# Performance work log

Measured on AMD Instinct MI355X. Metric: run time of the kernel, lower is better.

Reference implementation:

```python
import jax, jax.numpy as jnp
import numpy as np

H = 1024          # hidden_size
RH = 2 * H        # router/expert hidden (hidden_multiplier=2)
E = 3             # num_experts
B, T, P = 8, 2048, 64
LN_EPS = 1e-5


def _layer_norm(x, gamma, beta):
    mu = jnp.mean(x, axis=-1, keepdims=True)
    var = jnp.mean(jnp.square(x - mu), axis=-1, keepdims=True)
    return (x - mu) * jax.lax.rsqrt(var + LN_EPS) * gamma + beta


def setup_inputs() -> dict:
    key = jax.random.key(0)
    ks = jax.random.split(key, 24)
    s = lambda fan_in: 1.0 / np.sqrt(fan_in)
    inp = {
        "mix_hidden_states": jax.random.normal(ks[0], (B, T, H), jnp.float32),
        "global_anchor": jax.random.normal(ks[1], (B, H), jnp.float32),
        "prototype_bank": jax.random.normal(ks[2], (B, P, H), jnp.float32),
        # LayerNorm
        "ln_gamma": jnp.ones((H,), jnp.float32),
        "ln_beta": jnp.zeros((H,), jnp.float32),
        # retriever (no bias)
        "Wq": jax.random.normal(ks[3], (H, H), jnp.float32) * s(H),
        "Wk": jax.random.normal(ks[4], (H, H), jnp.float32) * s(H),
        "Wv": jax.random.normal(ks[5], (H, H), jnp.float32) * s(H),
        # router linear: 3H -> E
        "router_W": jax.random.normal(ks[6], (3 * H, E), jnp.float32) * s(3 * H),
        "router_b": jnp.zeros((E,), jnp.float32),
        # experts stacked: [E, 3H, RH] and [E, RH, H]
        "e_w1": jax.random.normal(ks[7], (E, 3 * H, RH), jnp.float32) * s(3 * H),
        "e_b1": jnp.zeros((E, RH), jnp.float32),
        "e_w2": jax.random.normal(ks[8], (E, RH, H), jnp.float32) * s(RH),
        "e_b2": jnp.zeros((E, H), jnp.float32),
        # gate MLP: 3H -> H -> H
        "gate_w1": jax.random.normal(ks[9], (3 * H, H), jnp.float32) * s(3 * H),
        "gate_b1": jnp.zeros((H,), jnp.float32),
        "gate_w2": jax.random.normal(ks[10], (H, H), jnp.float32) * s(H),
        "gate_b2": jnp.zeros((H,), jnp.float32),
        # out_proj (zero-init in torch, but use random for nontrivial baseline)
        "out_w": jax.random.normal(ks[11], (H, H), jnp.float32) * s(H),
        "out_b": jnp.zeros((H,), jnp.float32),
    }
    return inp


def reference(mix_hidden_states, global_anchor, prototype_bank,
              ln_gamma, ln_beta, Wq, Wk, Wv, router_W, router_b,
              e_w1, e_b1, e_w2, e_b2, gate_w1, gate_b1, gate_w2, gate_b2,
              out_w, out_b):
    x = mix_hidden_states
    nx = _layer_norm(x, ln_gamma, ln_beta)                      # [B,T,H]

    # --- evidence retriever (cross-attention over prototype bank) ---
    q = nx @ Wq                                                 # [B,T,H]
    k = prototype_bank @ Wk                                     # [B,P,H]
    v = prototype_bank @ Wv                                     # [B,P,H]
    scores = jnp.einsum('bth,bph->btp', q, k) * (H ** -0.5)
    weights = jax.nn.softmax(scores, axis=-1)
    evidence = jnp.einsum('btp,bph->bth', weights, v)           # [B,T,H]

    anchor = jnp.broadcast_to(global_anchor[:, None, :], nx.shape)
    combined = jnp.concatenate([nx, evidence, anchor], axis=-1) # [B,T,3H]

    # --- soft MoE router ---
    router_logits = combined @ router_W + router_b              # [B,T,E]
    router_probs = jax.nn.softmax(router_logits, axis=-1)
    h = jax.nn.silu(jnp.einsum('btc,ecr->bter', combined, e_w1) + e_b1)
    expert_out = jnp.einsum('bter,erh->bteh', h, e_w2) + e_b2   # [B,T,E,H]
    routed = jnp.sum(expert_out * router_probs[..., None], axis=-2)

    # --- sigmoid gate + residual ---
    g = jax.nn.sigmoid(jax.nn.silu(combined @ gate_w1 + gate_b1) @ gate_w2 + gate_b2)
    refined_delta = g * (routed @ out_w + out_b)
    return x + refined_delta
```

## Files before the change

kernel.cpp:

```cpp
#include <hip/hip_runtime.h>

typedef unsigned short u16;
typedef __bf16 bf16x8 __attribute__((ext_vector_type(8)));
typedef float f32x4 __attribute__((ext_vector_type(4)));

__device__ __forceinline__ float b2f(u16 u) {
  union { unsigned int i; float f; } x; x.i = ((unsigned int)u) << 16; return x.f;
}
__device__ __forceinline__ u16 f2b(float f) {
  union { float f; unsigned int i; } x; x.f = f;
  unsigned int r = (x.i + 0x7fffu + ((x.i >> 16) & 1u)) >> 16;
  return (u16)r;
}

__device__ __forceinline__ void async16(const void* g, void* l) {
  __builtin_amdgcn_global_load_lds((const __attribute__((address_space(1))) void*)g,
                                   (__attribute__((address_space(3))) void*)l, 16, 0, 0);
}

#define EPI_BF16    0
#define EPI_SILU    1
#define EPI_SIGMOID 2
#define EPI_ROUTED  3
#define EPI_FINAL   4
#define EPI_F32SC   5

__global__ __launch_bounds__(256) void gemm_bt(
    const u16* __restrict__ A, int lda, long long sA,
    const u16* __restrict__ B, int ldb, long long sB,
    const float* __restrict__ bias,
    const float* __restrict__ bcast, int ldbc,
    void* __restrict__ Cv, int ldc, long long sC,
    int M, int N, int K,
    int epi, float scale,
    const float* __restrict__ rowscale, int rs_off, int accum,
    const float* __restrict__ Xres, const u16* __restrict__ Gg)
{
  __shared__ u16 As[2][128 * 32];
  __shared__ u16 Bs[2][128 * 32];
  const int z = blockIdx.z;
  A += (long long)z * sA;
  B += (long long)z * sB;
  const int m0 = blockIdx.y * 128, n0 = blockIdx.x * 128;
  const int tid = threadIdx.x;
  const int lane = tid & 63, w = tid >> 6;
  const int wm = w >> 1, wn = w & 1;

  const int sr = lane >> 2;
  const int sc = (lane & 3) * 8;
  int ra0 = m0 + w * 16 + sr;      if (ra0 > M - 1) ra0 = M - 1;
  int ra1 = m0 + 64 + w * 16 + sr; if (ra1 > M - 1) ra1 = M - 1;
  int rb0 = n0 + w * 16 + sr;      if (rb0 > N - 1) rb0 = N - 1;
  int rb1 = n0 + 64 + w * 16 + sr; if (rb1 > N - 1) rb1 = N - 1;
  const u16* pa0 = A + (long long)ra0 * lda + sc;
  const u16* pa1 = A + (long long)ra1 * lda + sc;
  const u16* pb0 = B + (long long)rb0 * ldb + sc;
  const u16* pb1 = B + (long long)rb1 * ldb + sc;
  const int lw = w * 512;

  f32x4 acc[4][4] = {};

  const int kch = (lane >> 4) * 8;
  const int rr = lane & 15;

  async16(pa0, &As[0][lw]);
  async16(pa1, &As[0][2048 + lw]);
  async16(pb0, &Bs[0][lw]);
  async16(pb1, &Bs[0][2048 + lw]);

  int cur = 0;
  for (int k0 = 0; k0 < K; k0 += 32) {
    __syncthreads();
    const int kn = k0 + 32;
    if (kn < K) {
      const int nb = cur ^ 1;
      async16(pa0 + kn, &As[nb][lw]);
      async16(pa1 + kn, &As[nb][2048 + lw]);
      async16(pb0 + kn, &Bs[nb][lw]);
      async16(pb1 + kn, &Bs[nb][2048 + lw]);
    }
    bf16x8 af[4], bfr[4];
#pragma unroll
    for (int mi = 0; mi < 4; ++mi)
      af[mi] = *(const bf16x8*)(&As[cur][(wm * 64 + mi * 16 + rr) * 32 + kch]);
#pragma unroll
    for (int ni = 0; ni < 4; ++ni)
      bfr[ni] = *(const bf16x8*)(&Bs[cur][(wn * 64 + ni * 16 + rr) * 32 + kch]);
#pragma unroll
    for (int mi = 0; mi < 4; ++mi)
#pragma unroll
      for (int ni = 0; ni < 4; ++ni)
        acc[mi][ni] = __builtin_amdgcn_mfma_f32_16x16x32_bf16(af[mi], bfr[ni], acc[mi][ni], 0, 0, 0);
    cur ^= 1;
  }

  u16* Cb = (u16*)Cv;
  float* Cf = (float*)Cv;
#pragma unroll
  for (int ni = 0; ni < 4; ++ni) {
    int col = n0 + wn * 64 + ni * 16 + (lane & 15);
    if (col >= N) continue;
    float bv = bias ? bias[col] : 0.0f;
#pragma unroll
    for (int mi = 0; mi < 4; ++mi) {
#pragma unroll
      for (int r = 0; r < 4; ++r) {
        int row = m0 + wm * 64 + mi * 16 + (lane >> 4) * 4 + r;
        if (row >= M) continue;
        float v = acc[mi][ni][r] + bv;
        if (bcast) v += bcast[(row >> 11) * ldbc + col];
        long long cidx = (long long)z * sC + (long long)row * ldc + col;
        if (epi == EPI_BF16) {
          Cb[cidx] = f2b(v);
        } else if (epi == EPI_SILU) {
          Cb[cidx] = f2b(v / (1.0f + __expf(-v)));
        } else if (epi == EPI_SIGMOID) {
          Cb[cidx] = f2b(1.0f / (1.0f + __expf(-v)));
        } else if (epi == EPI_ROUTED) {
          float rs = rowscale[row * 3 + rs_off];
          if (accum) Cf[cidx] += rs * v; else Cf[cidx] = rs * v;
        } else if (epi == EPI_FINAL) {
          long long xi = (long long)row * ldc + col;
          Cf[cidx] = Xres[xi] + b2f(Gg[xi]) * v;
        } else {
          Cf[cidx] = v * scale;
        }
      }
    }
  }
}

__global__ __launch_bounds__(256) void transpose_cvt(const float* __restrict__ in, u16* __restrict__ out, int R, int C) {
  __shared__ float tile[32][33];
  int c0 = blockIdx.x * 32, r0 = blockIdx.y * 32;
  int tx = threadIdx.x & 31, ty = threadIdx.x >> 5;
#pragma unroll
  for (int i = 0; i < 4; ++i) {
    int r = ty + i * 8;
    tile[r][tx] = in[(long long)(r0 + r) * C + c0 + tx];
  }
  __syncthreads();
#pragma unroll
  for (int i = 0; i < 4; ++i) {
    int r = ty + i * 8;
    out[(long long)(c0 + r) * R + r0 + tx] = f2b(tile[tx][r]);
  }
}

__global__ __launch_bounds__(256) void cvt_bf16(const float* __restrict__ in, u16* __restrict__ out, int n) {
  for (int i = blockIdx.x * 256 + threadIdx.x; i < n; i += gridDim.x * 256)
    out[i] = f2b(in[i]);
}

__global__ __launch_bounds__(256) void ln_kernel(const float* __restrict__ x, const float* __restrict__ gamma,
                                                 const float* __restrict__ beta, u16* __restrict__ ne) {
  int t = blockIdx.x;
  int tid = threadIdx.x;
  const float* xr = x + (long long)t * 1024;
  float v[4];
  float s = 0.f, sq = 0.f;
#pragma unroll
  for (int i = 0; i < 4; ++i) {
    v[i] = xr[tid * 4 + i];
    s += v[i]; sq += v[i] * v[i];
  }
#pragma unroll
  for (int d = 32; d; d >>= 1) { s += __shfl_xor(s, d, 64); sq += __shfl_xor(sq, d, 64); }
  __shared__ float ls[4], lq[4];
  int w = tid >> 6, lane = tid & 63;
  if (lane == 0) { ls[w] = s; lq[w] = sq; }
  __syncthreads();
  s = ls[0] + ls[1] + ls[2] + ls[3];
  sq = lq[0] + lq[1] + lq[2] + lq[3];
  float mean = s * (1.0f / 1024.0f);
  float var = sq * (1.0f / 1024.0f) - mean * mean;
  float rstd = rsqrtf(var + 1e-5f);
  long long base = (long long)t * 2048;
#pragma unroll
  for (int i = 0; i < 4; ++i) {
    int c = tid * 4 + i;
    ne[base + c] = f2b((v[i] - mean) * rstd * gamma[c] + beta[c]);
  }
}

#define ANCH_KC 32
__global__ __launch_bounds__(256) void anchor_partial(const float* __restrict__ anchor, const float* __restrict__ W,
                                                      int ldw, int N, float* __restrict__ partial) {
  int n = blockIdx.x * 256 + threadIdx.x;
  if (n >= N) return;
  const int kc = blockIdx.y;
  const int kper = 1024 / ANCH_KC;
  const int k0 = kc * kper;
  float acc[8] = {};
  for (int k = k0; k < k0 + kper; ++k) {
    float wv = W[(long long)(2048 + k) * ldw + n];
#pragma unroll
    for (int b = 0; b < 8; ++b) acc[b] += anchor[b * 1024 + k] * wv;
  }
#pragma unroll
  for (int b = 0; b < 8; ++b)
    partial[((long long)kc * 8 + b) * N + n] = acc[b];
}

__global__ __launch_bounds__(256) void anchor_reduce(const float* __restrict__ partial, int N, float* __restrict__ bc) {
  int i = blockIdx.x * 256 + threadIdx.x;
  if (i >= 8 * N) return;
  float s = 0.f;
#pragma unroll 8
  for (int kc = 0; kc < ANCH_KC; ++kc) s += partial[(long long)kc * 8 * N + i];
  bc[i] = s;
}

__global__ __launch_bounds__(256) void attn_softmax(const float* __restrict__ scores, u16* __restrict__ weights) {
  int gid = blockIdx.x * 256 + threadIdx.x;
  int t = gid >> 6, lane = gid & 63;
  float sv = scores[(long long)t * 64 + lane];
  float m = sv;
#pragma unroll
  for (int d = 32; d; d >>= 1) m = fmaxf(m, __shfl_xor(m, d, 64));
  float e = __expf(sv - m);
  float sum = e;
#pragma unroll
  for (int d = 32; d; d >>= 1) sum += __shfl_xor(sum, d, 64);
  weights[(long long)t * 64 + lane] = f2b(e / sum);
}

__global__ __launch_bounds__(256) void router_kernel(const u16* __restrict__ ne, const float* __restrict__ anchor,
                                                     const float* __restrict__ rW, const float* __restrict__ rb,
                                                     float* __restrict__ probs) {
  int gid = blockIdx.x * 256 + threadIdx.x;
  int t = gid >> 6, lane = gid & 63;
  int b = t >> 11;
  const u16* cr = ne + (long long)t * 2048;
  const float* ar = anchor + (long long)b * 1024;
  float s0 = 0.f, s1 = 0.f, s2 = 0.f;
  for (int c = lane; c < 2048; c += 64) {
    float xv = b2f(cr[c]);
    s0 += xv * rW[c * 3 + 0];
    s1 += xv * rW[c * 3 + 1];
    s2 += xv * rW[c * 3 + 2];
  }
  for (int c = lane; c < 1024; c += 64) {
    float xv = ar[c];
    s0 += xv * rW[(2048 + c) * 3 + 0];
    s1 += xv * rW[(2048 + c) * 3 + 1];
    s2 += xv * rW[(2048 + c) * 3 + 2];
  }
#pragma unroll
  for (int d = 32; d; d >>= 1) {
    s0 += __shfl_xor(s0, d, 64);
    s1 += __shfl_xor(s1, d, 64);
    s2 += __shfl_xor(s2, d, 64);
  }
  s0 += rb[0]; s1 += rb[1]; s2 += rb[2];
  float m = fmaxf(s0, fmaxf(s1, s2));
  float e0 = __expf(s0 - m), e1 = __expf(s1 - m), e2 = __expf(s2 - m);
  float inv = 1.0f / (e0 + e1 + e2);
  if (lane == 0) {
    probs[(long long)t * 3 + 0] = e0 * inv;
    probs[(long long)t * 3 + 1] = e1 * inv;
    probs[(long long)t * 3 + 2] = e2 * inv;
  }
}

extern "C" void kernel_launch(void* const* d_in, const int* in_sizes, int n_in,
                              void* d_out, int out_size, void* d_ws, size_t ws_size,
                              hipStream_t stream) {
  const float* X      = (const float*)d_in[0];
  const float* anchor = (const float*)d_in[1];
  const float* proto  = (const float*)d_in[2];
  const float* gamma  = (const float*)d_in[3];
  const float* beta   = (const float*)d_in[4];
  const float* Wq     = (const float*)d_in[5];
  const float* Wk     = (const float*)d_in[6];
  const float* Wv     = (const float*)d_in[7];
  const float* rW     = (const float*)d_in[8];
  const float* rb     = (const float*)d_in[9];
  const float* ew1    = (const float*)d_in[10];
  const float* eb1    = (const float*)d_in[11];
  const float* ew2    = (const float*)d_in[12];
  const float* eb2    = (const float*)d_in[13];
  const float* gw1    = (const float*)d_in[14];
  const float* gb1    = (const float*)d_in[15];
  const float* gw2    = (const float*)d_in[16];
  const float* gb2    = (const float*)d_in[17];
  const float* ow     = (const float*)d_in[18];
  const float* ob     = (const float*)d_in[19];
  float* out = (float*)d_out;

  char* p = (char*)d_ws;
  size_t used = 0;
  auto alloc = [&](size_t bytes) {
    char* r = p; size_t a = (bytes + 255) & ~((size_t)255);
    p += a; used += a; return r;
  };
  u16* ne     = (u16*)alloc(16384ull * 2048 * 2);
  u16* S1     = (u16*)alloc(16384ull * 2048 * 2);
  float* routed = (float*)alloc(16384ull * 1024 * 4);
  u16* w8     = (u16*)alloc(2048ull * 2048 * 2);
  u16* proto_bf = (u16*)alloc(512ull * 1024 * 2);
  u16* kbuf   = (u16*)alloc(512ull * 1024 * 2);
  u16* v_t    = (u16*)alloc(1024ull * 512 * 2);
  u16* wts    = (u16*)alloc(16384ull * 64 * 2);
  float* scores = (float*)alloc(16384ull * 64 * 4);
  float* probs  = (float*)alloc(16384ull * 3 * 4);
  float* anch   = (float*)alloc(8ull * 2048 * 4);
  float* anchp  = (float*)alloc((size_t)ANCH_KC * 8 * 2048 * 4);
  if (used > ws_size) return;

  u16* gh = S1;
  u16* g  = S1 + 16384ull * 1024;
  u16* routed_bf = S1;

  auto gemm = [&](const u16* A, int lda, long long sA,
                  const u16* B, int ldb, long long sB,
                  const float* bias, const float* bcast, int ldbc,
                  void* C, int ldc, long long sC,
                  int M, int N, int K, int Z,
                  int epi, float scale, const float* rs, int rs_off, int accum,
                  const float* Xr, const u16* Gg) {
    dim3 grd((N + 127) / 128, (M + 127) / 128, Z);
    gemm_bt<<<grd, 256, 0, stream>>>(A, lda, sA, B, ldb, sB, bias, bcast, ldbc,
                                     C, ldc, sC, M, N, K, epi, scale, rs, rs_off, accum, Xr, Gg);
  };

  auto anchor_term = [&](const float* W, int ldw, int N, float* bc) {
    anchor_partial<<<dim3((N + 255) / 256, ANCH_KC), 256, 0, stream>>>(anchor, W, ldw, N, anchp);
    anchor_reduce<<<(8 * N + 255) / 256, 256, 0, stream>>>(anchp, N, bc);
  };

  ln_kernel<<<16384, 256, 0, stream>>>(X, gamma, beta, ne);
  cvt_bf16<<<512, 256, 0, stream>>>(proto, proto_bf, 512 * 1024);

  transpose_cvt<<<dim3(32, 32), 256, 0, stream>>>(Wk, w8, 1024, 1024);
  gemm(proto_bf, 1024, 0, w8, 1024, 0, nullptr, nullptr, 0, kbuf, 1024, 0,
       512, 1024, 1024, 1, EPI_BF16, 0.f, nullptr, 0, 0, nullptr, nullptr);

  transpose_cvt<<<dim3(32, 32), 256, 0, stream>>>(Wv, w8, 1024, 1024);
  gemm(w8, 1024, 0, proto_bf, 1024, 0, nullptr, nullptr, 0, v_t, 512, 0,
       1024, 512, 1024, 1, EPI_BF16, 0.f, nullptr, 0, 0, nullptr, nullptr);

  transpose_cvt<<<dim3(32, 32), 256, 0, stream>>>(Wq, w8, 1024, 1024);
  gemm(ne, 2048, 0, w8, 1024, 0, nullptr, nullptr, 0, S1, 1024, 0,
       16384, 1024, 1024, 1, EPI_BF16, 0.f, nullptr, 0, 0, nullptr, nullptr);

  gemm(S1, 1024, 2048ll * 1024, kbuf, 1024, 64ll * 1024, nullptr, nullptr, 0,
       scores, 64, 2048ll * 64, 2048, 64, 1024, 8, EPI_F32SC, 0.03125f, nullptr, 0, 0, nullptr, nullptr);
  attn_softmax<<<4096, 256, 0, stream>>>(scores, wts);
  gemm(wts, 64, 2048ll * 64, v_t, 512, 64, nullptr, nullptr, 0,
       ne + 1024, 2048, 2048ll * 2048, 2048, 1024, 64, 8, EPI_BF16, 0.f, nullptr, 0, 0, nullptr, nullptr);

  router_kernel<<<4096, 256, 0, stream>>>(ne, anchor, rW, rb, probs);

  for (int e = 0; e < 3; ++e) {
    const float* W1 = ew1 + (long long)e * 3072 * 2048;
    const float* W2 = ew2 + (long long)e * 2048 * 1024;
    transpose_cvt<<<dim3(64, 64), 256, 0, stream>>>(W1, w8, 2048, 2048);
    anchor_term(W1, 2048, 2048, anch);
    gemm(ne, 2048, 0, w8, 2048, 0, eb1 + e * 2048, anch, 2048, S1, 2048, 0,
         16384, 2048, 2048, 1, EPI_SILU, 0.f, nullptr, 0, 0, nullptr, nullptr);
    transpose_cvt<<<dim3(32, 64), 256, 0, stream>>>(W2, w8, 2048, 1024);
    gemm(S1, 2048, 0, w8, 2048, 0, eb2 + e * 1024, nullptr, 0, routed, 1024, 0,
         16384, 1024, 2048, 1, EPI_ROUTED, 0.f, probs, e, (e > 0) ? 1 : 0, nullptr, nullptr);
  }

  transpose_cvt<<<dim3(32, 64), 256, 0, stream>>>(gw1, w8, 2048, 1024);
  anchor_term(gw1, 1024, 1024, anch);
  gemm(ne, 2048, 0, w8, 2048, 0, gb1, anch, 1024, gh, 1024, 0,
       16384, 1024, 2048, 1, EPI_SILU, 0.f, nullptr, 0, 0, nullptr, nullptr);
  transpose_cvt<<<dim3(32, 32), 256, 0, stream>>>(gw2, w8, 1024, 1024);
  gemm(gh, 1024, 0, w8, 1024, 0, gb2, nullptr, 0, g, 1024, 0,
       16384, 1024, 1024, 1, EPI_SIGMOID, 0.f, nullptr, 0, 0, nullptr, nullptr);

  cvt_bf16<<<4096, 256, 0, stream>>>(routed, routed_bf, 16777216);
  transpose_cvt<<<dim3(32, 32), 256, 0, stream>>>(ow, w8, 1024, 1024);
  gemm(routed_bf, 1024, 0, w8, 1024, 0, ob, nullptr, 0, out, 1024, 0,
       16384, 1024, 1024, 1, EPI_FINAL, 0.f, nullptr, 0, 0, X, g);
}
```

Before: 2.140 ms.

## Add 256x256 tiled GEMM with async LDS pipelining for large GEMMs

Adds a new 512-thread GEMM kernel using 256x256 output tiles, 8 LDS slots with async global-to-LDS loads double-buffered across K steps, XOR-swizzled LDS layout, workgroup swizzling for L2 locality, and setprio around MFMA bursts. Large single-batch GEMMs dispatch to it while small or batched ones keep the old 128x128 kernel. The larger tile raises arithmetic intensity and overlaps loads with compute. In exchange it uses more registers and LDS per workgroup, and leaves fewer workgroups for some shapes.

Result: slower. 2.291 ms (+7.1%).

```diff
diff --git a/kernel.cpp b/kernel.cpp
--- a/kernel.cpp
+++ b/kernel.cpp
@@ -110,6 +110,170 @@
         float v = acc[mi][ni][r] + bv;
         if (bcast) v += bcast[(row >> 11) * ldbc + col];
         long long cidx = (long long)z * sC + (long long)row * ldc + col;
+        if (epi == EPI_BF16) {
+          Cb[cidx] = f2b(v);
+        } else if (epi == EPI_SILU) {
+          Cb[cidx] = f2b(v / (1.0f + __expf(-v)));
+        } else if (epi == EPI_SIGMOID) {
+          Cb[cidx] = f2b(1.0f / (1.0f + __expf(-v)));
+        } else if (epi == EPI_ROUTED) {
+          float rs = rowscale[row * 3 + rs_off];
+          if (accum) Cf[cidx] += rs * v; else Cf[cidx] = rs * v;
+        } else if (epi == EPI_FINAL) {
+          long long xi = (long long)row * ldc + col;
+          Cf[cidx] = Xres[xi] + b2f(Gg[xi]) * v;
+        } else {
+          Cf[cidx] = v * scale;
+        }
+      }
+    }
+  }
+}
+
+#define CFENCE asm volatile("" ::: "memory")
+
+#define STAGE(H, T_, SLOT) do { \
+  const u16* s_ = ((H) & 1) ? srcB : srcA; \
+  const long long ld_ = ((H) & 1) ? (long long)ldb : (long long)lda; \
+  const u16* p_ = s_ + (((H) >> 1) ? 128 * ld_ : 0) + (long long)(T_) * 64; \
+  u16* lb_ = &lds8[SLOT][w * 1024]; \
+  async16(p_, lb_); \
+  async16(p_ + 8 * ld_, lb_ + 512); \
+} while (0)
+
+#define READA(SLOT) do { \
+  _Pragma("unroll") for (int fm = 0; fm < 4; ++fm) { \
+    af[fm][0] = *(const bf16x8*)&lds8[SLOT][(wm * 64 + fm * 16 + rr) * 64 + cx0]; \
+    af[fm][1] = *(const bf16x8*)&lds8[SLOT][(wm * 64 + fm * 16 + rr) * 64 + cx1]; \
+  } } while (0)
+
+#define READB(SLOT) do { \
+  _Pragma("unroll") for (int fn = 0; fn < 2; ++fn) { \
+    bf[fn][0] = *(const bf16x8*)&lds8[SLOT][(wn * 32 + fn * 16 + rr) * 64 + cx0]; \
+    bf[fn][1] = *(const bf16x8*)&lds8[SLOT][(wn * 32 + fn * 16 + rr) * 64 + cx1]; \
+  } } while (0)
+
+#define MMAC(QM, QN) do { \
+  __builtin_amdgcn_s_setprio(1); \
+  _Pragma("unroll") for (int fm = 0; fm < 4; ++fm) { \
+    _Pragma("unroll") for (int fn = 0; fn < 2; ++fn) { \
+      acc[(QM)*4+fm][(QN)*2+fn] = __builtin_amdgcn_mfma_f32_16x16x32_bf16(af[fm][0], bf[fn][0], acc[(QM)*4+fm][(QN)*2+fn], 0, 0, 0); \
+      acc[(QM)*4+fm][(QN)*2+fn] = __builtin_amdgcn_mfma_f32_16x16x32_bf16(af[fm][1], bf[fn][1], acc[(QM)*4+fm][(QN)*2+fn], 0, 0, 0); \
+    } } \
+  __builtin_amdgcn_s_setprio(0); \
+} while (0)
+
+__global__ __launch_bounds__(512, 2) void gemm256_bt(
+    const u16* __restrict__ A, int lda,
+    const u16* __restrict__ B, int ldb,
+    const float* __restrict__ bias,
+    const float* __restrict__ bcast, int ldbc,
+    void* __restrict__ Cv, int ldc,
+    int M, int N, int K,
+    int epi, float scale,
+    const float* __restrict__ rowscale, int rs_off, int accum,
+    const float* __restrict__ Xres, const u16* __restrict__ Gg)
+{
+  __shared__ u16 lds8[8][8192];
+
+  int gx = gridDim.x;
+  int nwg = gx * gridDim.y;
+  int bid = blockIdx.y * gx + blockIdx.x;
+  int bx, by;
+  if ((nwg & 7) == 0) {
+    int cpx = nwg >> 3;
+    int swz = (bid & 7) * cpx + (bid >> 3);
+    bx = swz % gx; by = swz / gx;
+  } else { bx = blockIdx.x; by = blockIdx.y; }
+  const int m0 = by * 256, n0 = bx * 256;
+
+  const int tid = threadIdx.x;
+  const int lane = tid & 63, w = tid >> 6;
+  const int wm = w >> 2, wn = w & 3;
+  const int rr = lane & 15;
+
+  const int cx0 = (((lane >> 4) * 16)      ^ ((lane & 7) << 4)) >> 1;
+  const int cx1 = ((64 + (lane >> 4) * 16) ^ ((lane & 7) << 4)) >> 1;
+
+  const int rloc = w * 16 + (lane >> 3);
+  const int swz8 = 8 * ((lane & 7) ^ (lane >> 3));
+  const u16* srcA = A + (long long)(m0 + rloc) * lda + swz8;
+  const u16* srcB = B + (long long)(n0 + rloc) * ldb + swz8;
+
+  f32x4 acc[8][4] = {};
+  bf16x8 af[4][2], bf[2][2];
+
+  const int T = K >> 6;
+
+  STAGE(0, 0, 0); STAGE(1, 0, 1); STAGE(2, 0, 2); STAGE(3, 0, 3);
+  if (T > 1) { STAGE(0, 1, 4); STAGE(1, 1, 5); }
+  if (T > 1) { asm volatile("s_waitcnt vmcnt(4)" ::: "memory"); }
+  else       { asm volatile("s_waitcnt vmcnt(0)" ::: "memory"); }
+  __builtin_amdgcn_s_barrier();
+  CFENCE;
+
+  for (int s = 0; s < T; ++s) {
+    const int par = (s & 1) * 4;
+    const int opar = 4 - par;
+
+    READA(par + 0);
+    READB(par + 1);
+    CFENCE;
+    if (s + 1 < T) STAGE(2, s + 1, opar + 2);
+    __builtin_amdgcn_s_barrier();
+    CFENCE;
+    MMAC(0, 0);
+    __builtin_amdgcn_s_barrier();
+    CFENCE;
+
+    READB(par + 3);
+    CFENCE;
+    if (s + 1 < T) STAGE(3, s + 1, opar + 3);
+    __builtin_amdgcn_s_barrier();
+    CFENCE;
+    MMAC(0, 1);
+    __builtin_amdgcn_s_barrier();
+    CFENCE;
+
+    READA(par + 2);
+    READB(par + 1);
+    CFENCE;
+    if (s + 2 < T) STAGE(0, s + 2, par + 0);
+    __builtin_amdgcn_s_barrier();
+    CFENCE;
+    MMAC(1, 0);
+    __builtin_amdgcn_s_barrier();
+    CFENCE;
+
+    READB(par + 3);
+    CFENCE;
+    if (s + 2 < T) {
+      STAGE(1, s + 2, par + 1);
+      asm volatile("s_waitcnt vmcnt(4)" ::: "memory");
+    } else if (s + 1 < T) {
+      asm volatile("s_waitcnt vmcnt(0)" ::: "memory");
+    }
+    __builtin_amdgcn_s_barrier();
+    CFENCE;
+    MMAC(1, 1);
+    __builtin_amdgcn_s_barrier();
+    CFENCE;
+  }
+
+  u16* Cb = (u16*)Cv;
+  float* Cf = (float*)Cv;
+#pragma unroll
+  for (int ni = 0; ni < 4; ++ni) {
+    int col = n0 + (ni >> 1) * 128 + wn * 32 + (ni & 1) * 16 + (lane & 15);
+    float bv = bias ? bias[col] : 0.0f;
+#pragma unroll
+    for (int mi = 0; mi < 8; ++mi) {
+#pragma unroll
+      for (int r = 0; r < 4; ++r) {
+        int row = m0 + (mi >> 2) * 128 + wm * 64 + (mi & 3) * 16 + (lane >> 4) * 4 + r;
+        float v = acc[mi][ni][r] + bv;
+        if (bcast) v += bcast[(row >> 11) * ldbc + col];
+        long long cidx = (long long)row * ldc + col;
         if (epi == EPI_BF16) {
           Cb[cidx] = f2b(v);
         } else if (epi == EPI_SILU) {
@@ -319,9 +483,16 @@
                   int M, int N, int K, int Z,
                   int epi, float scale, const float* rs, int rs_off, int accum,
                   const float* Xr, const u16* Gg) {
-    dim3 grd((N + 127) / 128, (M + 127) / 128, Z);
-    gemm_bt<<<grd, 256, 0, stream>>>(A, lda, sA, B, ldb, sB, bias, bcast, ldbc,
-                                     C, ldc, sC, M, N, K, epi, scale, rs, rs_off, accum, Xr, Gg);
+    bool big = (Z == 1) && (M % 256 == 0) && (N % 256 == 0) && (K % 64 == 0) && (K >= 128) && (M >= 2048);
+    if (big) {
+      dim3 grd(N / 256, M / 256, 1);
+      gemm256_bt<<<grd, 512, 0, stream>>>(A, lda, B, ldb, bias, bcast, ldbc,
+                                          C, ldc, M, N, K, epi, scale, rs, rs_off, accum, Xr, Gg);
+    } else {
+      dim3 grd((N + 127) / 128, (M + 127) / 128, Z);
+      gemm_bt<<<grd, 256, 0, stream>>>(A, lda, sA, B, ldb, sB, bias, bcast, ldbc,
+                                       C, ldc, sC, M, N, K, epi, scale, rs, rs_off, accum, Xr, Gg);
+    }
   };
 
   auto anchor_term = [&](const float* W, int ldw, int N, float* bc) {
```
